# Kernel tuning notes

Measured on AMD Instinct MI355X. Metric: run time of the kernel, lower is better.

## Reference

```python
import jax, jax.numpy as jnp
import numpy as np

B = 64          # query batch
K = 4096        # anchor queue size (queue assumed full: ptr == K)
DIM = 50257     # vocab-sized distribution dim
KNN = 8
N_CLASS = 2
EPS = 1e-10


def setup_inputs() -> dict:
    key = jax.random.key(0)
    k1, k2, k3 = jax.random.split(key, 3)
    # anchors/queries are (unnormalized) positive distributions over the vocab
    query = jax.random.uniform(k1, (B, DIM), dtype=jnp.float32)
    queue_anchor = jax.random.uniform(k2, (K, DIM), dtype=jnp.float32)
    queue_label = jax.random.randint(k3, (K,), 0, N_CLASS)
    return {"query": query, "queue_anchor": queue_anchor, "queue_label": queue_label}


def reference(query, queue_anchor, queue_label):
    # enqueue() precomputes log(k_i) offline; reproduce that here
    queue_anchor_log = jnp.log(queue_anchor + EPS)          # [K, D]
    query_log = jnp.log(query + EPS)                        # [B, D]
    # kl[b,k] = mean_d a[k,d] * (alog[k,d] - qlog[b,d])
    #         = mean_d(a*alog)[k] - (1/D) * (qlog @ a^T)[b,k]
    # Same math as the original broadcast-then-mean, without materializing [B,K,D].
    self_term = jnp.mean(queue_anchor * queue_anchor_log, axis=1)      # [K]
    cross = jnp.einsum('bd,kd->bk', query_log, queue_anchor) / DIM     # [B, K]
    kl_distance = self_term[None, :] - cross                           # [B, K]
    # knn > 1 path: top-k smallest distances, then majority vote over labels
    _, indices = jax.lax.top_k(-kl_distance, KNN)                      # [B, KNN]
    knn_labels = queue_label[indices]                                  # [B, KNN]
    knn_cnt = jax.nn.one_hot(knn_labels, N_CLASS, dtype=jnp.float32).sum(axis=1)  # [B, n_class]
    return jnp.argmax(knn_cnt, axis=1)                                 # [B] int predictions
```

## Files before the change

### kernel.cpp

```cpp
#include <hip/hip_runtime.h>
#include <math.h>

#define B_Q   64
#define K_A   4096
#define DIMV  50257
#define KPAD  50688
#define NK    8
#define KCH   6336
#define DT    64
#define LR    72
#define TN    64

typedef short bf16x8 __attribute__((ext_vector_type(8)));
typedef float f32x4  __attribute__((ext_vector_type(4)));

static __device__ __forceinline__ unsigned short f2bf(float x) {
    unsigned int u = __builtin_bit_cast(unsigned int, x);
    unsigned int r = u + 0x7FFFu + ((u >> 16) & 1u);
    return (unsigned short)(r >> 16);
}
static __device__ __forceinline__ float bf2f(unsigned short h) {
    unsigned int u = ((unsigned int)h) << 16;
    return __builtin_bit_cast(float, u);
}

__global__ void qprep_k(const float* __restrict__ q,
                        unsigned short* __restrict__ qh,
                        unsigned short* __restrict__ ql) {
    int col = blockIdx.x * 256 + threadIdx.x;
    int row = blockIdx.y;
    float x = 0.f;
    if (col < DIMV) x = logf(q[row * DIMV + col] + 1e-10f);
    unsigned short h = f2bf(x);
    unsigned short l = f2bf(x - bf2f(h));
    qh[row * KPAD + col] = h;
    ql[row * KPAD + col] = l;
}

__global__ __launch_bounds__(256, 2)
void gemm_k(const unsigned short* __restrict__ qh_g,
            const unsigned short* __restrict__ ql_g,
            const float* __restrict__ anc,
            float* __restrict__ cpart, float* __restrict__ spart)
{
    __shared__ __align__(16) unsigned short qh_s[B_Q * LR];
    __shared__ __align__(16) unsigned short ql_s[B_Q * LR];
    __shared__ __align__(16) unsigned short ah_s[TN * LR];
    __shared__ __align__(16) unsigned short al_s[TN * LR];

    const int t    = threadIdx.x;
    const int n0   = blockIdx.x * TN;
    const int c    = blockIdx.y;
    const int lane = t & 63;
    const int m0   = (t >> 6) * 16;
    const int l15  = lane & 15;
    const int q4   = lane >> 4;

    f32x4 acc[4];
#pragma unroll
    for (int i = 0; i < 4; i++) acc[i] = (f32x4){0.f, 0.f, 0.f, 0.f};
    float sacc[4] = {0.f, 0.f, 0.f, 0.f};

    const int arow = t >> 4;
    const int ac4  = (t & 15) * 4;

    for (int kb = c * KCH; kb < (c + 1) * KCH; kb += DT) {
#pragma unroll
        for (int j = 0; j < 4; j++) {
            int idx = t + 256 * j;
            int sel = idx >> 9;
            int rem = idx & 511;
            int row = rem >> 3;
            int g   = rem & 7;
            const unsigned short* src = (sel ? ql_g : qh_g) + (size_t)row * KPAD + kb + g * 8;
            unsigned short* dst = (sel ? ql_s : qh_s) + row * LR + g * 8;
            *(uint4*)dst = *(const uint4*)src;
        }
        const bool full = (kb + DT <= DIMV);
#pragma unroll
        for (int j = 0; j < 4; j++) {
            const int r = arow + 16 * j;
            const int d = kb + ac4;
            const float* ap = anc + (size_t)(n0 + r) * DIMV + d;
            float a0, a1, a2, a3;
            if (full) {
                float4 v = *(const float4*)ap;
                a0 = v.x; a1 = v.y; a2 = v.z; a3 = v.w;
            } else {
                a0 = (d + 0 < DIMV) ? ap[0] : 0.f;
                a1 = (d + 1 < DIMV) ? ap[1] : 0.f;
                a2 = (d + 2 < DIMV) ? ap[2] : 0.f;
                a3 = (d + 3 < DIMV) ? ap[3] : 0.f;
            }
            sacc[j] += a0 * logf(a0 + 1e-10f) + a1 * logf(a1 + 1e-10f)
                     + a2 * logf(a2 + 1e-10f) + a3 * logf(a3 + 1e-10f);
            ushort4 hv, lv;
            hv.x = f2bf(a0); lv.x = f2bf(a0 - bf2f(hv.x));
            hv.y = f2bf(a1); lv.y = f2bf(a1 - bf2f(hv.y));
            hv.z = f2bf(a2); lv.z = f2bf(a2 - bf2f(hv.z));
            hv.w = f2bf(a3); lv.w = f2bf(a3 - bf2f(hv.w));
            *(ushort4*)(ah_s + r * LR + ac4) = hv;
            *(ushort4*)(al_s + r * LR + ac4) = lv;
        }
        __syncthreads();

#pragma unroll
        for (int ks = 0; ks < DT; ks += 32) {
            const int koff = ks + q4 * 8;
            bf16x8 a_h = *(const bf16x8*)(qh_s + (m0 + l15) * LR + koff);
            bf16x8 a_l = *(const bf16x8*)(ql_s + (m0 + l15) * LR + koff);
#pragma unroll
            for (int tl = 0; tl < 4; tl++) {
                bf16x8 b_h = *(const bf16x8*)(ah_s + (16 * tl + l15) * LR + koff);
                bf16x8 b_l = *(const bf16x8*)(al_s + (16 * tl + l15) * LR + koff);
                acc[tl] = __builtin_amdgcn_mfma_f32_16x16x32_bf16(a_h, b_h, acc[tl], 0, 0, 0);
                acc[tl] = __builtin_amdgcn_mfma_f32_16x16x32_bf16(a_h, b_l, acc[tl], 0, 0, 0);
                acc[tl] = __builtin_amdgcn_mfma_f32_16x16x32_bf16(a_l, b_h, acc[tl], 0, 0, 0);
            }
        }
        __syncthreads();
    }

#pragma unroll
    for (int tl = 0; tl < 4; tl++)
#pragma unroll
        for (int r = 0; r < 4; r++) {
            int m = m0 + q4 * 4 + r;
            int n = n0 + 16 * tl + l15;
            cpart[((size_t)(c * B_Q + m)) * K_A + n] = acc[tl][r];
        }

#pragma unroll
    for (int j = 0; j < 4; j++) {
        float s = sacc[j];
#pragma unroll
        for (int m = 1; m <= 8; m <<= 1) s += __shfl_xor(s, m, 64);
        if ((t & 15) == 0) spart[c * K_A + n0 + arow + 16 * j] = s;
    }
}

__global__ void topk_k(const float* __restrict__ cpart, const float* __restrict__ spart,
                       const int* __restrict__ labels, int* __restrict__ out)
{
    __shared__ float vals[K_A];
    __shared__ float rmin[256];
    __shared__ int   ridx[256];
    __shared__ int   chosen[8];

    const int b = blockIdx.x;
    const int t = threadIdx.x;

    for (int k = t; k < K_A; k += 256) {
        float s = 0.f, cr = 0.f;
#pragma unroll
        for (int c = 0; c < NK; c++) {
            s  += spart[c * K_A + k];
            cr += cpart[(size_t)(c * B_Q + b) * K_A + k];
        }
        vals[k] = s - cr;
    }
    __syncthreads();

    for (int it = 0; it < 8; it++) {
        float mv = INFINITY; int mi = 1 << 30;
        for (int k = t; k < K_A; k += 256) {
            float v = vals[k];
            if (v < mv) { mv = v; mi = k; }
        }
        rmin[t] = mv; ridx[t] = mi;
        __syncthreads();
        for (int s = 128; s > 0; s >>= 1) {
            if (t < s) {
                float v2 = rmin[t + s]; int i2 = ridx[t + s];
                if (v2 < rmin[t] || (v2 == rmin[t] && i2 < ridx[t])) {
                    rmin[t] = v2; ridx[t] = i2;
                }
            }
            __syncthreads();
        }
        if (t == 0) { chosen[it] = ridx[0]; vals[ridx[0]] = INFINITY; }
        __syncthreads();
    }

    if (t == 0) {
        int cnt1 = 0;
#pragma unroll
        for (int it = 0; it < 8; it++) cnt1 += labels[chosen[it]];
        out[b] = (cnt1 >= 5) ? 1 : 0;
    }
}

extern "C" void kernel_launch(void* const* d_in, const int* in_sizes, int n_in,
                              void* d_out, int out_size, void* d_ws, size_t ws_size,
                              hipStream_t stream) {
    const float* query  = (const float*)d_in[0];
    const float* anchor = (const float*)d_in[1];
    const int*   labels = (const int*)d_in[2];
    int* out = (int*)d_out;

    char* ws = (char*)d_ws;
    unsigned short* qh = (unsigned short*)ws;
    unsigned short* ql = (unsigned short*)(ws + 6488064);
    float* cpart = (float*)(ws + 12976128);
    float* spart = (float*)(ws + 12976128 + 8388608);

    qprep_k<<<dim3(KPAD / 256, B_Q), 256, 0, stream>>>(query, qh, ql);
    gemm_k<<<dim3(K_A / TN, NK), 256, 0, stream>>>(qh, ql, anchor, cpart, spart);
    topk_k<<<B_Q, 256, 0, stream>>>(cpart, spart, labels, out);
}
```

Baseline: 1.352 ms.

## Software-pipeline anchor loads, keep query fragments in registers, split K into 12 chunks

The GEMM kernel now prefetches the next 64-column anchor tile and the query fragments into registers while it computes the current one. It uses double-buffered LDS with a single barrier per stage and loads the query operand straight from global memory into registers instead of staging it in shared memory. It also raises the K-split to 12 chunks, asks for 3 blocks per CU, remaps block IDs so neighbouring blocks share a K chunk, and replaces logf with a log2-based fast log. The top-k kernel swaps its shared-memory tree reduction for wave shuffles. These changes aim to hide global-load latency and cut barrier overhead, at the cost of more register pressure, a larger partial-sum buffer and slightly lower log precision.

Measured after the change: 1.213 ms. 1.11x faster.

```diff
diff --git a/kernel.cpp b/kernel.cpp
--- a/kernel.cpp
+++ b/kernel.cpp
@@ -5,9 +5,10 @@
 #define K_A   4096
 #define DIMV  50257
 #define KPAD  50688
-#define NK    8
-#define KCH   6336
+#define NK    12
+#define KCH   4224
 #define DT    64
+#define NSTG  66
 #define LR    72
 #define TN    64
 
@@ -22,6 +23,9 @@
 static __device__ __forceinline__ float bf2f(unsigned short h) {
     unsigned int u = ((unsigned int)h) << 16;
     return __builtin_bit_cast(float, u);
+}
+static __device__ __forceinline__ float fastln(float x) {
+    return __log2f(x) * 0.69314718055994531f;
 }
 
 __global__ void qprep_k(const float* __restrict__ q,
@@ -30,27 +34,28 @@
     int col = blockIdx.x * 256 + threadIdx.x;
     int row = blockIdx.y;
     float x = 0.f;
-    if (col < DIMV) x = logf(q[row * DIMV + col] + 1e-10f);
+    if (col < DIMV) x = logf(q[(size_t)row * DIMV + col] + 1e-10f);
     unsigned short h = f2bf(x);
     unsigned short l = f2bf(x - bf2f(h));
-    qh[row * KPAD + col] = h;
-    ql[row * KPAD + col] = l;
-}
-
-__global__ __launch_bounds__(256, 2)
+    qh[(size_t)row * KPAD + col] = h;
+    ql[(size_t)row * KPAD + col] = l;
+}
+
+__global__ __launch_bounds__(256, 3)
 void gemm_k(const unsigned short* __restrict__ qh_g,
             const unsigned short* __restrict__ ql_g,
             const float* __restrict__ anc,
             float* __restrict__ cpart, float* __restrict__ spart)
 {
-    __shared__ __align__(16) unsigned short qh_s[B_Q * LR];
-    __shared__ __align__(16) unsigned short ql_s[B_Q * LR];
-    __shared__ __align__(16) unsigned short ah_s[TN * LR];
-    __shared__ __align__(16) unsigned short al_s[TN * LR];
+    __shared__ __align__(16) unsigned short ah_s[2][TN * LR];
+    __shared__ __align__(16) unsigned short al_s[2][TN * LR];
+
+    const int F  = blockIdx.x + (K_A / TN) * blockIdx.y;
+    const int wg = (F & 7) * 96 + (F >> 3);
+    const int c  = wg >> 6;
+    const int n0 = (wg & 63) * TN;
 
     const int t    = threadIdx.x;
-    const int n0   = blockIdx.x * TN;
-    const int c    = blockIdx.y;
     const int lane = t & 63;
     const int m0   = (t >> 6) * 16;
     const int l15  = lane & 15;
@@ -63,79 +68,110 @@
 
     const int arow = t >> 4;
     const int ac4  = (t & 15) * 4;
-
-    for (int kb = c * KCH; kb < (c + 1) * KCH; kb += DT) {
+    const int kb0  = c * KCH;
+
+    const unsigned short* qph = qh_g + (size_t)(m0 + l15) * KPAD + kb0 + q4 * 8;
+    const unsigned short* qpl = ql_g + (size_t)(m0 + l15) * KPAD + kb0 + q4 * 8;
+
+    bf16x8 qfh0 = *(const bf16x8*)(qph);
+    bf16x8 qfh1 = *(const bf16x8*)(qph + 32);
+    bf16x8 qfl0 = *(const bf16x8*)(qpl);
+    bf16x8 qfl1 = *(const bf16x8*)(qpl + 32);
+    float4 av[4];
+#pragma unroll
+    for (int j = 0; j < 4; j++) {
+        const float* ap = anc + (size_t)(n0 + arow + 16 * j) * DIMV + kb0 + ac4;
+        av[j] = *(const float4*)ap;
+    }
+
+#pragma unroll 1
+    for (int s = 0; s < NSTG; ++s) {
+        const int p = s & 1;
+        const bool have_next = (s + 1 < NSTG);
+
+        bf16x8 nqh0, nqh1, nql0, nql1;
+        float4 nv[4];
+        if (have_next) {
+            const int off = (s + 1) * DT;
+            nqh0 = *(const bf16x8*)(qph + off);
+            nqh1 = *(const bf16x8*)(qph + off + 32);
+            nql0 = *(const bf16x8*)(qpl + off);
+            nql1 = *(const bf16x8*)(qpl + off + 32);
+            const int kbn = kb0 + off;
+            const bool fullN = (kbn + DT <= DIMV);
+#pragma unroll
+            for (int j = 0; j < 4; j++) {
+                const float* ap = anc + (size_t)(n0 + arow + 16 * j) * DIMV + kbn + ac4;
+                if (fullN) {
+                    nv[j] = *(const float4*)ap;
+                } else {
+                    const int d = kbn + ac4;
+                    nv[j].x = (d + 0 < DIMV) ? ap[0] : 0.f;
+                    nv[j].y = (d + 1 < DIMV) ? ap[1] : 0.f;
+                    nv[j].z = (d + 2 < DIMV) ? ap[2] : 0.f;
+                    nv[j].w = (d + 3 < DIMV) ? ap[3] : 0.f;
+                }
+            }
+        }
+
 #pragma unroll
         for (int j = 0; j < 4; j++) {
-            int idx = t + 256 * j;
-            int sel = idx >> 9;
-            int rem = idx & 511;
-            int row = rem >> 3;
-            int g   = rem & 7;
-            const unsigned short* src = (sel ? ql_g : qh_g) + (size_t)row * KPAD + kb + g * 8;
-            unsigned short* dst = (sel ? ql_s : qh_s) + row * LR + g * 8;
-            *(uint4*)dst = *(const uint4*)src;
-        }
-        const bool full = (kb + DT <= DIMV);
-#pragma unroll
-        for (int j = 0; j < 4; j++) {
-            const int r = arow + 16 * j;
-            const int d = kb + ac4;
-            const float* ap = anc + (size_t)(n0 + r) * DIMV + d;
-            float a0, a1, a2, a3;
-            if (full) {
-                float4 v = *(const float4*)ap;
-                a0 = v.x; a1 = v.y; a2 = v.z; a3 = v.w;
-            } else {
-                a0 = (d + 0 < DIMV) ? ap[0] : 0.f;
-                a1 = (d + 1 < DIMV) ? ap[1] : 0.f;
-                a2 = (d + 2 < DIMV) ? ap[2] : 0.f;
-                a3 = (d + 3 < DIMV) ? ap[3] : 0.f;
-            }
-            sacc[j] += a0 * logf(a0 + 1e-10f) + a1 * logf(a1 + 1e-10f)
-                     + a2 * logf(a2 + 1e-10f) + a3 * logf(a3 + 1e-10f);
+            const float a0 = av[j].x, a1 = av[j].y, a2 = av[j].z, a3 = av[j].w;
+            sacc[j] += a0 * fastln(a0 + 1e-10f) + a1 * fastln(a1 + 1e-10f)
+                     + a2 * fastln(a2 + 1e-10f) + a3 * fastln(a3 + 1e-10f);
             ushort4 hv, lv;
             hv.x = f2bf(a0); lv.x = f2bf(a0 - bf2f(hv.x));
             hv.y = f2bf(a1); lv.y = f2bf(a1 - bf2f(hv.y));
             hv.z = f2bf(a2); lv.z = f2bf(a2 - bf2f(hv.z));
             hv.w = f2bf(a3); lv.w = f2bf(a3 - bf2f(hv.w));
-            *(ushort4*)(ah_s + r * LR + ac4) = hv;
-            *(ushort4*)(al_s + r * LR + ac4) = lv;
+            const int r = arow + 16 * j;
+            *(ushort4*)(&ah_s[p][r * LR + ac4]) = hv;
+            *(ushort4*)(&al_s[p][r * LR + ac4]) = lv;
         }
         __syncthreads();
 
-#pragma unroll
-        for (int ks = 0; ks < DT; ks += 32) {
-            const int koff = ks + q4 * 8;
-            bf16x8 a_h = *(const bf16x8*)(qh_s + (m0 + l15) * LR + koff);
-            bf16x8 a_l = *(const bf16x8*)(ql_s + (m0 + l15) * LR + koff);
+        {
+            const int k0 = q4 * 8;
 #pragma unroll
             for (int tl = 0; tl < 4; tl++) {
-                bf16x8 b_h = *(const bf16x8*)(ah_s + (16 * tl + l15) * LR + koff);
-                bf16x8 b_l = *(const bf16x8*)(al_s + (16 * tl + l15) * LR + koff);
-                acc[tl] = __builtin_amdgcn_mfma_f32_16x16x32_bf16(a_h, b_h, acc[tl], 0, 0, 0);
-                acc[tl] = __builtin_amdgcn_mfma_f32_16x16x32_bf16(a_h, b_l, acc[tl], 0, 0, 0);
-                acc[tl] = __builtin_amdgcn_mfma_f32_16x16x32_bf16(a_l, b_h, acc[tl], 0, 0, 0);
+                bf16x8 b_h = *(const bf16x8*)(&ah_s[p][(16 * tl + l15) * LR + k0]);
+                bf16x8 b_l = *(const bf16x8*)(&al_s[p][(16 * tl + l15) * LR + k0]);
+                acc[tl] = __builtin_amdgcn_mfma_f32_16x16x32_bf16(qfh0, b_h, acc[tl], 0, 0, 0);
+                acc[tl] = __builtin_amdgcn_mfma_f32_16x16x32_bf16(qfh0, b_l, acc[tl], 0, 0, 0);
+                acc[tl] = __builtin_amdgcn_mfma_f32_16x16x32_bf16(qfl0, b_h, acc[tl], 0, 0, 0);
             }
-        }
-        __syncthreads();
+#pragma unroll
+            for (int tl = 0; tl < 4; tl++) {
+                bf16x8 b_h = *(const bf16x8*)(&ah_s[p][(16 * tl + l15) * LR + 32 + k0]);
+                bf16x8 b_l = *(const bf16x8*)(&al_s[p][(16 * tl + l15) * LR + 32 + k0]);
+                acc[tl] = __builtin_amdgcn_mfma_f32_16x16x32_bf16(qfh1, b_h, acc[tl], 0, 0, 0);
+                acc[tl] = __builtin_amdgcn_mfma_f32_16x16x32_bf16(qfh1, b_l, acc[tl], 0, 0, 0);
+                acc[tl] = __builtin_amdgcn_mfma_f32_16x16x32_bf16(qfl1, b_h, acc[tl], 0, 0, 0);
+            }
+        }
+
+        if (have_next) {
+#pragma unroll
+            for (int j = 0; j < 4; j++) av[j] = nv[j];
+            qfh0 = nqh0; qfh1 = nqh1; qfl0 = nql0; qfl1 = nql1;
+        }
     }
 
 #pragma unroll
     for (int tl = 0; tl < 4; tl++)
 #pragma unroll
         for (int r = 0; r < 4; r++) {
-            int m = m0 + q4 * 4 + r;
-            int n = n0 + 16 * tl + l15;
+            const int m = m0 + q4 * 4 + r;
+            const int n = n0 + 16 * tl + l15;
             cpart[((size_t)(c * B_Q + m)) * K_A + n] = acc[tl][r];
         }
 
 #pragma unroll
     for (int j = 0; j < 4; j++) {
-        float s = sacc[j];
-#pragma unroll
-        for (int m = 1; m <= 8; m <<= 1) s += __shfl_xor(s, m, 64);
-        if ((t & 15) == 0) spart[c * K_A + n0 + arow + 16 * j] = s;
+        float sum = sacc[j];
+#pragma unroll
+        for (int m = 1; m <= 8; m <<= 1) sum += __shfl_xor(sum, m, 64);
+        if ((t & 15) == 0) spart[c * K_A + n0 + arow + 16 * j] = sum;
     }
 }
 
@@ -143,12 +179,13 @@
                        const int* __restrict__ labels, int* __restrict__ out)
 {
     __shared__ float vals[K_A];
-    __shared__ float rmin[256];
-    __shared__ int   ridx[256];
+    __shared__ float wmv[4];
+    __shared__ int   wmi[4];
     __shared__ int   chosen[8];
 
     const int b = blockIdx.x;
     const int t = threadIdx.x;
+    const int w = t >> 6, lane = t & 63;
 
     for (int k = t; k < K_A; k += 256) {
         float s = 0.f, cr = 0.f;
@@ -167,18 +204,22 @@
             float v = vals[k];
             if (v < mv) { mv = v; mi = k; }
         }
-        rmin[t] = mv; ridx[t] = mi;
+#pragma unroll
+        for (int m = 1; m <= 32; m <<= 1) {
+            float v2 = __shfl_xor(mv, m, 64);
+            int   i2 = __shfl_xor(mi, m, 64);
+            if (v2 < mv || (v2 == mv && i2 < mi)) { mv = v2; mi = i2; }
+        }
+        if (lane == 0) { wmv[w] = mv; wmi[w] = mi; }
         __syncthreads();
-        for (int s = 128; s > 0; s >>= 1) {
-            if (t < s) {
-                float v2 = rmin[t + s]; int i2 = ridx[t + s];
-                if (v2 < rmin[t] || (v2 == rmin[t] && i2 < ridx[t])) {
-                    rmin[t] = v2; ridx[t] = i2;
-                }
-            }
-            __syncthreads();
-        }
-        if (t == 0) { chosen[it] = ridx[0]; vals[ridx[0]] = INFINITY; }
+        if (t == 0) {
+            float bv = wmv[0]; int bi = wmi[0];
+#pragma unroll
+            for (int i = 1; i < 4; i++)
+                if (wmv[i] < bv || (wmv[i] == bv && wmi[i] < bi)) { bv = wmv[i]; bi = wmi[i]; }
+            chosen[it] = bi;
+            vals[bi] = INFINITY;
+        }
         __syncthreads();
     }
 
@@ -202,7 +243,7 @@
     unsigned short* qh = (unsigned short*)ws;
     unsigned short* ql = (unsigned short*)(ws + 6488064);
     float* cpart = (float*)(ws + 12976128);
-    float* spart = (float*)(ws + 12976128 + 8388608);
+    float* spart = (float*)(ws + 12976128 + 12582912);
 
     qprep_k<<<dim3(KPAD / 256, B_Q), 256, 0, stream>>>(query, qh, ql);
     gemm_k<<<dim3(K_A / TN, NK), 256, 0, stream>>>(qh, ql, anchor, cpart, spart);
```
